# Optimization experiments

Hardware: AMD Instinct MI355X
Metric: run time of the kernel (lower is better)

The kernel has to match this reference:

```python
import jax, jax.numpy as jnp
import numpy as np

B, C, L, K = 64, 2, 131072, 4


def setup_inputs() -> dict:
    key = jax.random.key(0)
    k1, k2, k3, k4 = jax.random.split(key, 4)
    x = jax.random.normal(k1, (B, C, L), dtype=jnp.float32)
    Bs = 0.5 * jax.random.normal(k2, (B, C, K, 3), dtype=jnp.float32)
    # Build stable denominators: complex-conjugate poles r*exp(+-j*theta), r < 0.95
    # a(z) = 1 - 2 r cos(theta) z^-1 + r^2 z^-2  -> guaranteed-stable IIR cascade.
    r = jax.random.uniform(k3, (B, C, K), minval=0.1, maxval=0.95)
    theta = jax.random.uniform(k4, (B, C, K), minval=0.05, maxval=np.pi - 0.05)
    a1 = -2.0 * r * jnp.cos(theta)
    a2 = r * r
    As = jnp.stack([jnp.ones_like(a1), a1, a2], axis=-1).astype(jnp.float32)
    return {"input_signal": x, "Bs": Bs, "As": As}


def _biquad_cascade(x, b, a):
    # x: [N, L]; b, a: [N, K, 3] with a already normalized (a0 == 1).
    # Serial cascade of K biquads, each in direct form II transposed:
    #   y[n]  = b0*u[n] + s1
    #   s1'   = b1*u[n] - a1*y[n] + s2
    #   s2'   = b2*u[n] - a2*y[n]
    # Exactly the linear recurrence the ssm/lfilter backends compute.
    nK = b.shape[1]
    b0, b1, b2 = b[..., 0], b[..., 1], b[..., 2]  # each [N, K]
    a1, a2 = a[..., 1], a[..., 2]

    def step(carry, xt):
        s1, s2 = carry  # each [N, K]
        u = xt  # [N]
        s1n, s2n = [], []
        for k in range(nK):  # small fixed cascade depth, unrolled
            y = b0[:, k] * u + s1[:, k]
            s1n.append(b1[:, k] * u - a1[:, k] * y + s2[:, k])
            s2n.append(b2[:, k] * u - a2[:, k] * y)
            u = y
        return (jnp.stack(s1n, axis=1), jnp.stack(s2n, axis=1)), u

    N = x.shape[0]
    init = (jnp.zeros((N, nK), x.dtype), jnp.zeros((N, nK), x.dtype))
    _, ys = jax.lax.scan(step, init, x.T)  # scan over time: ys [L, N]
    return ys.T


def reference(input_signal, Bs, As):
    b, c, audio_len = input_signal.shape
    assert Bs.shape[-1] == As.shape[-1] == 3
    # channel broadcasting as in _process_ssm
    if c == 1 and Bs.shape[1] > 1:
        input_signal = jnp.broadcast_to(input_signal, (b, Bs.shape[1], audio_len))
        c = Bs.shape[1]
    elif Bs.shape[1] == 1 and c > 1:
        Bs = jnp.broadcast_to(Bs, (b, c) + Bs.shape[2:])
        As = jnp.broadcast_to(As, (b, c) + As.shape[2:])
    a0 = As[..., :1]
    Bn = (Bs / a0).reshape(b * c, -1, 3)
    An = (As / a0).reshape(b * c, -1, 3)
    x = input_signal.reshape(b * c, audio_len)
    y = _biquad_cascade(x, Bn, An)
    return y.reshape(b, c, audio_len)
```

## Files before the change

kernel.cpp:

```cpp
#include <hip/hip_runtime.h>
#include <math.h>


#define SS   64
#define WMAX 384
#define WMIN 64
#define TT   32
#define TPB  256
#define CPB  512
#define LSTR 33
#define KB   4
#define NL   16

typedef float vf4 __attribute__((ext_vector_type(4)));
typedef float vf2 __attribute__((ext_vector_type(2)));

static __device__ __forceinline__ vf2 vfma2(vf2 a, vf2 b, vf2 c) {
    return __builtin_elementwise_fma(a, b, c);
}

__global__ void iir_prep_kernel(const float* __restrict__ As, int rows,
                                int* __restrict__ wrow, int* __restrict__ perm)
{
    __shared__ int sw[256];
    const int r = threadIdx.x;
    int W = 0;
    if (r < rows) {
        float r2max = 0.f;
#pragma unroll
        for (int k = 0; k < KB; ++k) {
            float a0 = As[(size_t)r * KB * 3 + 3 * k];
            float a2 = As[(size_t)r * KB * 3 + 3 * k + 2] / a0;
            r2max = fmaxf(r2max, a2);
        }
        float rmax = fminf(fmaxf(sqrtf(fmaxf(r2max, 0.f)), 0.20f), 0.955f);
        float Wf = 22.0f / (-logf(rmax));
        W = ((int)ceilf(Wf) + TT - 1) & ~(TT - 1);
        W = min(max(W, WMIN), WMAX);
        wrow[r] = W;
    }
    sw[r] = W;
    __syncthreads();
    if (r < rows) {
        int rank = 0;
        for (int i = 0; i < rows; ++i)
            rank += (sw[i] > W) || (sw[i] == W && i < r);
        perm[rank] = r;
    }
}

__global__ __launch_bounds__(TPB, 2) void iir_chunks_kernel(
    const float* __restrict__ x, const float* __restrict__ Bs,
    const float* __restrict__ As, float* __restrict__ out, int L,
    const int* __restrict__ wrow, const int* __restrict__ perm)
{
    __shared__ float lds[CPB * LSTR];
    const int tid = threadIdx.x;
    const int bpr = (L / SS) / CPB;
    const int row = perm[blockIdx.x / bpr];
    const int chunk0 = (blockIdx.x % bpr) * CPB;
    const int W = wrow[row];

    vf2 b0[KB], b1[KB], b2[KB], na1[KB], na2[KB];
    const float* Bp = Bs + (size_t)row * KB * 3;
    const float* Ap = As + (size_t)row * KB * 3;
#pragma unroll
    for (int k = 0; k < KB; ++k) {
        float inv = 1.0f / Ap[3 * k];
        float c0 =  Bp[3 * k]     * inv;
        float c1 =  Bp[3 * k + 1] * inv;
        float c2 =  Bp[3 * k + 2] * inv;
        float n1 = -Ap[3 * k + 1] * inv;
        float n2 = -Ap[3 * k + 2] * inv;
        b0[k] = vf2{c0, c0}; b1[k] = vf2{c1, c1}; b2[k] = vf2{c2, c2};
        na1[k] = vf2{n1, n1}; na2[k] = vf2{n2, n2};
    }

    vf2 s1[KB], s2[KB];
#pragma unroll
    for (int k = 0; k < KB; ++k) { s1[k] = vf2{0.f, 0.f}; s2[k] = vf2{0.f, 0.f}; }

    const float* xrow = x   + (size_t)row * L;
    float*       orow = out + (size_t)row * L;
    float*       r0 = lds + tid * LSTR;
    float*       r1 = r0 + 256 * LSTR;

    const int tq = tid >> 3;
    const int p4 = (tid & 7) << 2;
    int off[NL];
    int ldsoff[NL];
#pragma unroll
    for (int l = 0; l < NL; ++l) {
        int j = l * 32 + tq;
        off[l]    = (chunk0 + j) * SS + p4 - W;
        ldsoff[l] = j * LSTR + p4;
    }

    const int NT = (SS + W) / TT;
    const int WT = W / TT;
    const bool edge = (chunk0 == 0);

    float4 rn[NL];
    if (edge) {
#pragma unroll
        for (int l = 0; l < NL; ++l) {
            int pos = off[l];
            rn[l] = make_float4(0.f, 0.f, 0.f, 0.f);
            if (pos >= 0) rn[l] = *reinterpret_cast<const float4*>(xrow + pos);
        }
    } else {
#pragma unroll
        for (int l = 0; l < NL; ++l)
            rn[l] = *reinterpret_cast<const float4*>(xrow + off[l]);
    }

#pragma unroll 1
    for (int it = 0; it < NT; ++it) {
        __syncthreads();

#pragma unroll
        for (int l = 0; l < NL; ++l) {
            float* d = lds + ldsoff[l];
            d[0] = rn[l].x; d[1] = rn[l].y; d[2] = rn[l].z; d[3] = rn[l].w;
        }

        if (it + 1 < NT) {
            const int base = (it + 1) * TT;
            if (edge) {
#pragma unroll
                for (int l = 0; l < NL; ++l) {
                    int pos = off[l] + base;
                    rn[l] = make_float4(0.f, 0.f, 0.f, 0.f);
                    if (pos >= 0) rn[l] = *reinterpret_cast<const float4*>(xrow + pos);
                }
            } else {
#pragma unroll
                for (int l = 0; l < NL; ++l)
                    rn[l] = *reinterpret_cast<const float4*>(xrow + off[l] + base);
            }
        }

        __syncthreads();

        if (it < WT) {
#pragma unroll
            for (int p = 0; p < TT; ++p) {
                vf2 u = vf2{r0[p], r1[p]};
#pragma unroll
                for (int k = 0; k < KB; ++k) {
                    vf2 yv = vfma2(b0[k], u, s1[k]);
                    s1[k] = vfma2(na1[k], yv, vfma2(b1[k], u, s2[k]));
                    s2[k] = vfma2(na2[k], yv, b2[k] * u);
                    u = yv;
                }
            }
        } else {
#pragma unroll
            for (int p = 0; p < TT; ++p) {
                vf2 u = vf2{r0[p], r1[p]};
#pragma unroll
                for (int k = 0; k < KB; ++k) {
                    vf2 yv = vfma2(b0[k], u, s1[k]);
                    s1[k] = vfma2(na1[k], yv, vfma2(b1[k], u, s2[k]));
                    s2[k] = vfma2(na2[k], yv, b2[k] * u);
                    u = yv;
                }
                r0[p] = u.x; r1[p] = u.y;
            }
            __syncthreads();

            const int base = it * TT;
#pragma unroll
            for (int l = 0; l < NL; ++l) {
                const float* sp = lds + ldsoff[l];
                vf4 v = {sp[0], sp[1], sp[2], sp[3]};
                __builtin_nontemporal_store(
                    v, reinterpret_cast<vf4*>(orow + off[l] + base));
            }
        }
    }
}

extern "C" void kernel_launch(void* const* d_in, const int* in_sizes, int n_in,
                              void* d_out, int out_size, void* d_ws, size_t ws_size,
                              hipStream_t stream) {
    const float* x  = (const float*)d_in[0];
    const float* Bs = (const float*)d_in[1];
    const float* As = (const float*)d_in[2];
    float* out = (float*)d_out;

    const int rows = in_sizes[1] / (KB * 3);
    const int L    = in_sizes[0] / rows;
    const int bpr  = (L / SS) / CPB;

    int* wrow = (int*)d_ws;
    int* perm = wrow + rows;

    hipLaunchKernelGGL(iir_prep_kernel, dim3(1), dim3(256), 0, stream,
                       As, rows, wrow, perm);
    hipLaunchKernelGGL(iir_chunks_kernel, dim3(rows * bpr), dim3(TPB), 0, stream,
                       x, Bs, As, out, L, wrow, perm);
}
```

Measured before the change: 152.1 us.

## Replace LDS-staged chunk transpose with direct per-thread strided global loads and stores

Removes the shared-memory staging and the block-wide barriers. Each thread now loads its two chunks directly from global memory in 16-float units, double-buffered in registers, and writes its outputs straight back. Block size and chunks per block are halved to match. This drops the LDS traffic and synchronisation, but each lane's global accesses are now strided by the chunk size (256 bytes apart), which makes coalescing much worse than the old transposed layout.

Result: slower. 292.1 us (+92.1%).

```diff
diff --git a/kernel.cpp b/kernel.cpp
--- a/kernel.cpp
+++ b/kernel.cpp
@@ -5,12 +5,10 @@
 #define SS   64
 #define WMAX 384
 #define WMIN 64
-#define TT   32
-#define TPB  256
-#define CPB  512
-#define LSTR 33
+#define UT   16
+#define TPB  128
+#define CPB  256
 #define KB   4
-#define NL   16
 
 typedef float vf4 __attribute__((ext_vector_type(4)));
 typedef float vf2 __attribute__((ext_vector_type(2)));
@@ -35,7 +33,7 @@
         }
         float rmax = fminf(fmaxf(sqrtf(fmaxf(r2max, 0.f)), 0.20f), 0.955f);
         float Wf = 22.0f / (-logf(rmax));
-        W = ((int)ceilf(Wf) + TT - 1) & ~(TT - 1);
+        W = ((int)ceilf(Wf) + 31) & ~31;
         W = min(max(W, WMIN), WMAX);
         wrow[r] = W;
     }
@@ -49,12 +47,11 @@
     }
 }
 
-__global__ __launch_bounds__(TPB, 2) void iir_chunks_kernel(
+__global__ __launch_bounds__(TPB) void iir_direct_kernel(
     const float* __restrict__ x, const float* __restrict__ Bs,
     const float* __restrict__ As, float* __restrict__ out, int L,
     const int* __restrict__ wrow, const int* __restrict__ perm)
 {
-    __shared__ float lds[CPB * LSTR];
     const int tid = threadIdx.x;
     const int bpr = (L / SS) / CPB;
     const int row = perm[blockIdx.x / bpr];
@@ -82,70 +79,45 @@
 
     const float* xrow = x   + (size_t)row * L;
     float*       orow = out + (size_t)row * L;
-    float*       r0 = lds + tid * LSTR;
-    float*       r1 = r0 + 256 * LSTR;
 
-    const int tq = tid >> 3;
-    const int p4 = (tid & 7) << 2;
-    int off[NL];
-    int ldsoff[NL];
+    const int c0 = chunk0 + tid;
+    const int c1 = c0 + TPB;
+    const int base0 = c0 * SS - W;
+    const int base1 = c1 * SS - W;
+    const int NU = (W + SS) / UT;
+    const int NW = W / UT;
+
+    vf4 Ua[4], Ub[4], Va[4], Vb[4];
+
+    auto load_unit = [&](vf4* A, vf4* B, int s) {
+        const int o = s * UT;
+        if (base0 >= 0) {
 #pragma unroll
-    for (int l = 0; l < NL; ++l) {
-        int j = l * 32 + tq;
-        off[l]    = (chunk0 + j) * SS + p4 - W;
-        ldsoff[l] = j * LSTR + p4;
-    }
-
-    const int NT = (SS + W) / TT;
-    const int WT = W / TT;
-    const bool edge = (chunk0 == 0);
-
-    float4 rn[NL];
-    if (edge) {
+            for (int q = 0; q < 4; ++q)
+                A[q] = *reinterpret_cast<const vf4*>(xrow + base0 + o + q * 4);
+        } else {
 #pragma unroll
-        for (int l = 0; l < NL; ++l) {
-            int pos = off[l];
-            rn[l] = make_float4(0.f, 0.f, 0.f, 0.f);
-            if (pos >= 0) rn[l] = *reinterpret_cast<const float4*>(xrow + pos);
-        }
-    } else {
-#pragma unroll
-        for (int l = 0; l < NL; ++l)
-            rn[l] = *reinterpret_cast<const float4*>(xrow + off[l]);
-    }
-
-#pragma unroll 1
-    for (int it = 0; it < NT; ++it) {
-        __syncthreads();
-
-#pragma unroll
-        for (int l = 0; l < NL; ++l) {
-            float* d = lds + ldsoff[l];
-            d[0] = rn[l].x; d[1] = rn[l].y; d[2] = rn[l].z; d[3] = rn[l].w;
-        }
-
-        if (it + 1 < NT) {
-            const int base = (it + 1) * TT;
-            if (edge) {
-#pragma unroll
-                for (int l = 0; l < NL; ++l) {
-                    int pos = off[l] + base;
-                    rn[l] = make_float4(0.f, 0.f, 0.f, 0.f);
-                    if (pos >= 0) rn[l] = *reinterpret_cast<const float4*>(xrow + pos);
-                }
-            } else {
-#pragma unroll
-                for (int l = 0; l < NL; ++l)
-                    rn[l] = *reinterpret_cast<const float4*>(xrow + off[l] + base);
+            for (int q = 0; q < 4; ++q) {
+                int o0 = base0 + o + q * 4;
+                vf4 v = {0.f, 0.f, 0.f, 0.f};
+                if (o0 >= 0) v = *reinterpret_cast<const vf4*>(xrow + o0);
+                A[q] = v;
             }
         }
+#pragma unroll
+        for (int q = 0; q < 4; ++q)
+            B[q] = *reinterpret_cast<const vf4*>(xrow + base1 + o + q * 4);
+    };
 
-        __syncthreads();
-
-        if (it < WT) {
+    auto compute_unit = [&](vf4* A, vf4* B, int s) {
+        const bool outu = (s >= NW);
+        const int o = s * UT;
 #pragma unroll
-            for (int p = 0; p < TT; ++p) {
-                vf2 u = vf2{r0[p], r1[p]};
+        for (int q = 0; q < 4; ++q) {
+            vf4 ya, yb;
+#pragma unroll
+            for (int e = 0; e < 4; ++e) {
+                vf2 u = vf2{A[q][e], B[q][e]};
 #pragma unroll
                 for (int k = 0; k < KB; ++k) {
                     vf2 yv = vfma2(b0[k], u, s1[k]);
@@ -153,31 +125,26 @@
                     s2[k] = vfma2(na2[k], yv, b2[k] * u);
                     u = yv;
                 }
+                ya[e] = u.x; yb[e] = u.y;
             }
-        } else {
-#pragma unroll
-            for (int p = 0; p < TT; ++p) {
-                vf2 u = vf2{r0[p], r1[p]};
-#pragma unroll
-                for (int k = 0; k < KB; ++k) {
-                    vf2 yv = vfma2(b0[k], u, s1[k]);
-                    s1[k] = vfma2(na1[k], yv, vfma2(b1[k], u, s2[k]));
-                    s2[k] = vfma2(na2[k], yv, b2[k] * u);
-                    u = yv;
-                }
-                r0[p] = u.x; r1[p] = u.y;
-            }
-            __syncthreads();
-
-            const int base = it * TT;
-#pragma unroll
-            for (int l = 0; l < NL; ++l) {
-                const float* sp = lds + ldsoff[l];
-                vf4 v = {sp[0], sp[1], sp[2], sp[3]};
+            if (outu) {
                 __builtin_nontemporal_store(
-                    v, reinterpret_cast<vf4*>(orow + off[l] + base));
+                    ya, reinterpret_cast<vf4*>(orow + base0 + o + q * 4));
+                __builtin_nontemporal_store(
+                    yb, reinterpret_cast<vf4*>(orow + base1 + o + q * 4));
             }
         }
+    };
+
+    load_unit(Ua, Ub, 0);
+    load_unit(Va, Vb, 1);
+
+#pragma unroll 1
+    for (int s = 0; s < NU; s += 2) {
+        compute_unit(Ua, Ub, s);
+        if (s + 2 < NU) load_unit(Ua, Ub, s + 2);
+        compute_unit(Va, Vb, s + 1);
+        if (s + 3 < NU) load_unit(Va, Vb, s + 3);
     }
 }
 
@@ -198,6 +165,6 @@
 
     hipLaunchKernelGGL(iir_prep_kernel, dim3(1), dim3(256), 0, stream,
                        As, rows, wrow, perm);
-    hipLaunchKernelGGL(iir_chunks_kernel, dim3(rows * bpr), dim3(TPB), 0, stream,
+    hipLaunchKernelGGL(iir_direct_kernel, dim3(rows * bpr), dim3(TPB), 0, stream,
                        x, Bs, As, out, L, wrow, perm);
 }
```
